# Performance work log

Hardware: AMD Instinct MI355X
Metric: run time of the kernel (lower is better)

The kernel has to match this reference:

```python
import jax, jax.numpy as jnp
import numpy as np

RES = 14          # window resolution -> N = RES*RES = 196
NUM_HEADS = 24
HEAD_DIM = 32
DIM = NUM_HEADS * HEAD_DIM  # 768
CPB_HIDDEN = 512
BATCH = 128


def _swin2_table_index(res):
    """Swin-v2 continuous relative position bias: log-spaced coords table
    [(2r-1)^2, 2] and relative position index [N*N] (numpy, static)."""
    r = res
    coords = np.arange(-(r - 1), r, dtype=np.float32)
    table = np.stack(np.meshgrid(coords, coords, indexing="ij"), axis=-1)  # [2r-1, 2r-1, 2]
    table = table / (r - 1)  # pretrained_window_size == window_size
    table = table * 8.0
    table = np.sign(table) * np.log2(np.abs(table) + 1.0) / np.log2(8.0)
    table = table.reshape(-1, 2)

    grid = np.stack(np.meshgrid(np.arange(r), np.arange(r), indexing="ij"))  # [2, r, r]
    grid = grid.reshape(2, -1)  # [2, N]
    rel = grid[:, :, None] - grid[:, None, :]  # [2, N, N]
    rel = rel.transpose(1, 2, 0).astype(np.int64)  # [N, N, 2]
    rel[..., 0] += r - 1
    rel[..., 1] += r - 1
    rel[..., 0] *= 2 * r - 1
    index = rel.sum(-1).reshape(-1)  # [N*N]
    return table, index


def setup_inputs() -> dict:
    key = jax.random.key(0)
    ks = jax.random.split(key, 5)
    N = RES * RES
    x = jax.random.normal(ks[0], (BATCH, N, DIM), dtype=jnp.float32)
    qkv_w = jax.random.normal(ks[1], (DIM, 3 * DIM), dtype=jnp.float32) * (DIM ** -0.5)
    qkv_b = jnp.zeros((3 * DIM,), dtype=jnp.float32)
    proj_w = jax.random.normal(ks[2], (DIM, DIM), dtype=jnp.float32) * (DIM ** -0.5)
    proj_b = jnp.zeros((DIM,), dtype=jnp.float32)
    cpb_w1 = jax.random.normal(ks[3], (2, CPB_HIDDEN), dtype=jnp.float32) * (2 ** -0.5)
    cpb_b1 = jnp.zeros((CPB_HIDDEN,), dtype=jnp.float32)
    cpb_w2 = jax.random.normal(ks[4], (CPB_HIDDEN, NUM_HEADS), dtype=jnp.float32) * (CPB_HIDDEN ** -0.5)
    cpb_b2 = jnp.zeros((NUM_HEADS,), dtype=jnp.float32)
    return {"x": x, "qkv_w": qkv_w, "qkv_b": qkv_b, "proj_w": proj_w,
            "proj_b": proj_b, "cpb_w1": cpb_w1, "cpb_b1": cpb_b1,
            "cpb_w2": cpb_w2, "cpb_b2": cpb_b2}


def reference(x, qkv_w, qkv_b, proj_w, proj_b, cpb_w1, cpb_b1, cpb_w2, cpb_b2):
    B, N, C = x.shape
    H, hd = NUM_HEADS, HEAD_DIM

    table_np, index_np = _swin2_table_index(RES)
    table = jnp.asarray(table_np)            # [(2r-1)^2, 2]
    index = jnp.asarray(index_np)            # [N*N] int

    # qkv projection -> (3, B, H, N, hd)
    qkv = x @ qkv_w + qkv_b
    qkv = qkv.reshape(B, N, 3, H, hd).transpose(2, 0, 3, 1, 4)
    q, k, v = qkv[0], qkv[1], qkv[2]

    # scaled QK^T
    attn = jnp.einsum("bhnd,bhmd->bhnm", q, k) / jnp.sqrt(jnp.float32(hd))

    # continuous relative position bias: MLP(2->512->H), gather, 16*sigmoid
    h1 = jax.nn.relu(table @ cpb_w1 + cpb_b1)           # [(2r-1)^2, 512]
    bias_table = h1 @ cpb_w2 + cpb_b2                    # [(2r-1)^2, H]
    bias = bias_table[index].reshape(N, N, H).transpose(2, 0, 1)  # [H, N, N]
    bias = 16.0 * jax.nn.sigmoid(bias)

    attn = jax.nn.softmax(attn + bias[None], axis=-1)

    out = jnp.einsum("bhnm,bhmd->bhnd", attn, v)
    out = out.transpose(0, 2, 1, 3).reshape(B, N, C)
    out = out @ proj_w + proj_b
    return out
```

## Files before the change

kernel.cpp:

```cpp
#include <hip/hip_runtime.h>
#include <hip/hip_bf16.h>

typedef unsigned short u16;
typedef __attribute__((ext_vector_type(8))) short short8;
typedef __attribute__((ext_vector_type(8))) u16 u16x8;
typedef __attribute__((ext_vector_type(4))) u16 u16x4;
typedef __attribute__((ext_vector_type(4))) float f32x4;

__device__ __forceinline__ u16 f2bf(float f) {
  __hip_bfloat16 h = __float2bfloat16(f);
  u16 u;
  __builtin_memcpy(&u, &h, 2);
  return u;
}

__device__ __forceinline__ f32x4 mfma16(short8 a, short8 b, f32x4 c) {
  return __builtin_amdgcn_mfma_f32_16x16x32_bf16(a, b, c, 0, 0, 0);
}

__device__ __forceinline__ void gl_lds16(const void* g, void* l) {
  __builtin_amdgcn_global_load_lds(
      (const __attribute__((address_space(1))) unsigned int*)g,
      (__attribute__((address_space(3))) unsigned int*)l, 16, 0, 0);
}

__global__ __launch_bounds__(256) void cvt_x_k(const float* __restrict__ x,
                                               u16* __restrict__ xb) {
  int i = (blockIdx.x * 256 + threadIdx.x) * 4;
  float4 v = *(const float4*)(x + i);
  u16x4 o = { f2bf(v.x), f2bf(v.y), f2bf(v.z), f2bf(v.w) };
  *(u16x4*)(xb + i) = o;
}

__global__ __launch_bounds__(256) void cvt_wt_k(const float* __restrict__ w,
                                                u16* __restrict__ wt, int N) {
  int i = blockIdx.x * 256 + threadIdx.x;
  int nn = i / 768, kk = i % 768;
  wt[i] = f2bf(w[(size_t)kk * N + nn]);
}

__device__ __forceinline__ float cpb_coord(int v) {
  float c = (float)(v - 13) * (8.0f / 13.0f);
  float a = fabsf(c);
  float r = log2f(a + 1.0f) * (1.0f / 3.0f);
  return c < 0.f ? -r : r;
}

__global__ __launch_bounds__(64) void bias_mlp_k(
    const float* __restrict__ w1, const float* __restrict__ b1,
    const float* __restrict__ w2, const float* __restrict__ b2,
    float* __restrict__ btab) {
  int e = blockIdx.x;
  int lane = threadIdx.x;
  float t0 = cpb_coord(e / 27), t1 = cpb_coord(e % 27);
  float acc[24];
#pragma unroll
  for (int hh = 0; hh < 24; hh++) acc[hh] = 0.f;
#pragma unroll
  for (int jj = 0; jj < 8; jj++) {
    int j = lane * 8 + jj;
    float h1 = t0 * w1[j] + t1 * w1[512 + j] + b1[j];
    h1 = fmaxf(h1, 0.f);
#pragma unroll
    for (int hh = 0; hh < 24; hh++) acc[hh] += h1 * w2[j * 24 + hh];
  }
#pragma unroll
  for (int hh = 0; hh < 24; hh++)
#pragma unroll
    for (int m = 1; m < 64; m <<= 1) acc[hh] += __shfl_xor(acc[hh], m, 64);
  if (lane == 0) {
#pragma unroll
    for (int hh = 0; hh < 24; hh++) {
      float v = acc[hh] + b2[hh];
      btab[e * 24 + hh] = 16.f / (1.f + __expf(-v));
    }
  }
}

__global__ __launch_bounds__(256) void bias_expand_k(const float* __restrict__ tab,
                                                     float* __restrict__ be) {
  int i = blockIdx.x * 256 + threadIdx.x;
  int h = i / (196 * 208);
  int rem = i % (196 * 208);
  int row = rem / 208, col = rem % 208;
  float v = 0.f;
  if (col < 196) {
    int dy = row / 14 - col / 14 + 13;
    int dx = row % 14 - col % 14 + 13;
    v = tab[(dy * 27 + dx) * 24 + h];
  }
  be[i] = v;
}

template <int EPI>
__global__ __launch_bounds__(256) void gemm_k(
    const u16* __restrict__ A, const u16* __restrict__ Bt,
    const float* __restrict__ bias, float* __restrict__ Cf,
    u16* __restrict__ Cb, int N, int K, int nbx) {
  __shared__ u16 As[128 * 64];
  __shared__ u16 Bs[128 * 64];
  const int tid = threadIdx.x, lane = tid & 63, w = tid >> 6;
  const int r16 = lane & 15, q4 = lane >> 4;
  const int wr = w >> 1, wc = w & 1;
  const int nwg = gridDim.x, cpx = nwg >> 3;
  const int swz = (blockIdx.x & 7) * cpx + (blockIdx.x >> 3);
  const int m0 = (swz / nbx) * 128, n0 = (swz % nbx) * 128;

  f32x4 acc[4][4] = {};

  for (int k0 = 0; k0 < K; k0 += 64) {
#pragma unroll
    for (int g = 0; g < 4; g++) {
      int chunk = (w * 4 + g) * 64 + lane;
      int row = chunk >> 3, p = chunk & 7;
      int gch = p ^ (row & 7);
      gl_lds16(A + (size_t)(m0 + row) * K + k0 + gch * 8, (char*)As + (w * 4 + g) * 1024);
      gl_lds16(Bt + (size_t)(n0 + row) * K + k0 + gch * 8, (char*)Bs + (w * 4 + g) * 1024);
    }
    __syncthreads();
#pragma unroll
    for (int kk = 0; kk < 2; kk++) {
      short8 af[4], bfr[4];
#pragma unroll
      for (int i = 0; i < 4; i++) {
        int row = wr * 64 + i * 16 + r16;
        int pc = (kk * 4 + q4) ^ (r16 & 7);
        af[i] = *(const short8*)((const char*)As + row * 128 + pc * 16);
      }
#pragma unroll
      for (int j = 0; j < 4; j++) {
        int row = wc * 64 + j * 16 + r16;
        int pc = (kk * 4 + q4) ^ (r16 & 7);
        bfr[j] = *(const short8*)((const char*)Bs + row * 128 + pc * 16);
      }
#pragma unroll
      for (int i = 0; i < 4; i++)
#pragma unroll
        for (int j = 0; j < 4; j++) acc[i][j] = mfma16(af[i], bfr[j], acc[i][j]);
    }
    __syncthreads();
  }

  const int nb = n0 + wc * 64 + r16;
  float bn[4];
#pragma unroll
  for (int j = 0; j < 4; j++) bn[j] = bias[nb + j * 16];
#pragma unroll
  for (int i = 0; i < 4; i++) {
#pragma unroll
    for (int r = 0; r < 4; r++) {
      int m = m0 + wr * 64 + i * 16 + q4 * 4 + r;
      if (EPI == 1) {
        float* cp = Cf + (size_t)m * N + nb;
#pragma unroll
        for (int j = 0; j < 4; j++) cp[j * 16] = acc[i][j][r] + bn[j];
      } else {
        u16* cp = Cb + (size_t)m * N + nb;
#pragma unroll
        for (int j = 0; j < 4; j++) cp[j * 16] = f2bf(acc[i][j][r] + bn[j]);
      }
    }
  }
}

__global__ __launch_bounds__(256) void attn_k(
    const u16* __restrict__ qkv, const float* __restrict__ be,
    u16* __restrict__ ao) {
  constexpr int PST = 232, VST = 232;
  __shared__ u16 Ks[208 * 32];
  __shared__ u16 Vt[32 * VST];
  __shared__ u16 Ps[4][16 * PST];
  const int tid = threadIdx.x, lane = tid & 63, w = tid >> 6;
  const int r16 = lane & 15, q4 = lane >> 4;
  const int bh = blockIdx.x, b = bh / 24, h = bh % 24;
  const u16* qp = qkv + (size_t)(b * 196) * 2304 + h * 32;
  const u16* kp = qp + 768;
  const u16* vp = qp + 1536;
  const float* bp = be + h * (196 * 208);
  const int ksw = (q4 ^ ((r16 >> 1) & 3)) * 16;

  for (int g = w; g < 13; g += 4) {
    int chunk = g * 64 + lane;
    int row = chunk >> 2;
    int gch = (chunk & 3) ^ ((row >> 1) & 3);
    gl_lds16(kp + (size_t)row * 2304 + gch * 8, (char*)Ks + g * 1024);
  }
  for (int c = tid; c < 784; c += 256) {
    int n = c >> 2, d0 = (c & 3) * 8;
    u16x8 vv = *(const u16x8*)(vp + (size_t)n * 2304 + (c & 3) * 8);
#pragma unroll
    for (int jj = 0; jj < 8; jj++) Vt[(d0 + jj) * VST + n] = vv[jj];
  }
  for (int idx = tid; idx < 32 * 36; idx += 256) {
    int d = idx / 36, n = 196 + idx % 36;
    Vt[d * VST + n] = 0;
  }
  for (int idx = lane; idx < 16 * 24; idx += 64) {
    int row = idx / 24, col = 208 + idx % 24;
    Ps[w][row * PST + col] = 0;
  }
  __syncthreads();

  f32x4 z = {0.f, 0.f, 0.f, 0.f};
  for (int si = w; si < 13; si += 4) {
    short8 aq = *(const short8*)(qp + (size_t)(si * 16 + r16) * 2304 + q4 * 8);
    f32x4 acc[13];
#pragma unroll
    for (int t = 0; t < 13; t++) {
      short8 bk = *(const short8*)((const char*)Ks + (t * 16 + r16) * 64 + ksw);
      acc[t] = mfma16(aq, bk, z);
    }
    float mx[4] = {-3e38f, -3e38f, -3e38f, -3e38f};
#pragma unroll
    for (int t = 0; t < 13; t++) {
      int col = t * 16 + r16;
#pragma unroll
      for (int r = 0; r < 4; r++) {
        int grow = si * 16 + q4 * 4 + r;
        int gc = grow < 196 ? grow : 195;
        float s = acc[t][r] * 0.17677669529663687f + bp[gc * 208 + col];
        s = (col < 196) ? s : -3e38f;
        acc[t][r] = s;
        mx[r] = fmaxf(mx[r], s);
      }
    }
#pragma unroll
    for (int r = 0; r < 4; r++)
#pragma unroll
      for (int m = 1; m < 16; m <<= 1) mx[r] = fmaxf(mx[r], __shfl_xor(mx[r], m, 64));
    float sum[4] = {0.f, 0.f, 0.f, 0.f};
#pragma unroll
    for (int t = 0; t < 13; t++)
#pragma unroll
      for (int r = 0; r < 4; r++) {
        float p = __expf(acc[t][r] - mx[r]);
        acc[t][r] = p;
        sum[r] += p;
      }
#pragma unroll
    for (int r = 0; r < 4; r++) {
#pragma unroll
      for (int m = 1; m < 16; m <<= 1) sum[r] += __shfl_xor(sum[r], m, 64);
      sum[r] = 1.0f / sum[r];
    }
#pragma unroll
    for (int t = 0; t < 13; t++) {
      int col = t * 16 + r16;
#pragma unroll
      for (int r = 0; r < 4; r++)
        Ps[w][(q4 * 4 + r) * PST + col] = f2bf(acc[t][r] * sum[r]);
    }
    f32x4 o0 = z, o1 = z;
#pragma unroll
    for (int t = 0; t < 7; t++) {
      short8 ap = *(const short8*)(&Ps[w][r16 * PST + t * 32 + q4 * 8]);
      short8 b0 = *(const short8*)(&Vt[r16 * VST + t * 32 + q4 * 8]);
      short8 b1 = *(const short8*)(&Vt[(16 + r16) * VST + t * 32 + q4 * 8]);
      o0 = mfma16(ap, b0, o0);
      o1 = mfma16(ap, b1, o1);
    }
#pragma unroll
    for (int r = 0; r < 4; r++) {
      int grow = si * 16 + q4 * 4 + r;
      if (grow < 196) {
        u16* op = ao + ((size_t)(b * 196 + grow)) * 768 + h * 32;
        op[r16] = f2bf(o0[r]);
        op[16 + r16] = f2bf(o1[r]);
      }
    }
  }
}

extern "C" void kernel_launch(void* const* d_in, const int* in_sizes, int n_in,
                              void* d_out, int out_size, void* d_ws, size_t ws_size,
                              hipStream_t stream) {
  const float* x = (const float*)d_in[0];
  const float* qkv_w = (const float*)d_in[1];
  const float* qkv_b = (const float*)d_in[2];
  const float* proj_w = (const float*)d_in[3];
  const float* proj_b = (const float*)d_in[4];
  const float* cpb_w1 = (const float*)d_in[5];
  const float* cpb_b1 = (const float*)d_in[6];
  const float* cpb_w2 = (const float*)d_in[7];
  const float* cpb_b2 = (const float*)d_in[8];
  float* out = (float*)d_out;

  char* ws = (char*)d_ws;
  size_t o = 0;
  auto alloc = [&](size_t sz) {
    size_t r = o;
    o = (o + sz + 255) & ~(size_t)255;
    return r;
  };
  const size_t ME = (size_t)25088 * 768;
  u16* x_bf = (u16*)(ws + alloc(ME * 2));
  u16* wq_t = (u16*)(ws + alloc((size_t)2304 * 768 * 2));
  u16* wp_t = (u16*)(ws + alloc((size_t)768 * 768 * 2));
  u16* qkv_s = (u16*)(ws + alloc(3 * ME * 2));
  float* btab = (float*)(ws + alloc((size_t)729 * 24 * 4));
  float* bexp = (float*)(ws + alloc((size_t)24 * 196 * 208 * 4));
  u16* ao = x_bf;

  cvt_x_k<<<18816, 256, 0, stream>>>(x, x_bf);
  cvt_wt_k<<<6912, 256, 0, stream>>>(qkv_w, wq_t, 2304);
  cvt_wt_k<<<2304, 256, 0, stream>>>(proj_w, wp_t, 768);
  bias_mlp_k<<<729, 64, 0, stream>>>(cpb_w1, cpb_b1, cpb_w2, cpb_b2, btab);
  bias_expand_k<<<3822, 256, 0, stream>>>(btab, bexp);
  gemm_k<0><<<3528, 256, 0, stream>>>(x_bf, wq_t, qkv_b, nullptr, qkv_s,
                                      2304, 768, 18);
  attn_k<<<3072, 256, 0, stream>>>(qkv_s, bexp, ao);
  gemm_k<1><<<1176, 256, 0, stream>>>(ao, wp_t, proj_b, out, nullptr,
                                      768, 768, 6);
}
```

Baseline: 314.7 us.

## Keep softmax probabilities in registers via transposed QK^T and 16x16x16 MFMA for PV

The QK^T MFMA now computes S^T by swapping the operands, so each lane holds four consecutive key columns of one query row. The probabilities can then be fed directly as the A operand of 16x16x16 bf16 MFMAs for the PV product, which removes the per-wave LDS staging buffer and its round trip. The bias is pre-scaled by log2(e) so softmax uses exp2, the row reductions need only two shuffles, bias reads become float4 loads, and the attention kernel gets an occupancy hint in its launch bounds. The trade-offs are twice as many, smaller MFMAs for PV and a changed V padding stride, and the asm fallback for the MFMA builtin may be fragile.

```diff
diff --git a/kernel.cpp b/kernel.cpp
--- a/kernel.cpp
+++ b/kernel.cpp
@@ -3,6 +3,7 @@
 
 typedef unsigned short u16;
 typedef __attribute__((ext_vector_type(8))) short short8;
+typedef __attribute__((ext_vector_type(4))) short short4v;
 typedef __attribute__((ext_vector_type(8))) u16 u16x8;
 typedef __attribute__((ext_vector_type(4))) u16 u16x4;
 typedef __attribute__((ext_vector_type(4))) float f32x4;
@@ -16,6 +17,15 @@
 
 __device__ __forceinline__ f32x4 mfma16(short8 a, short8 b, f32x4 c) {
   return __builtin_amdgcn_mfma_f32_16x16x32_bf16(a, b, c, 0, 0, 0);
+}
+
+__device__ __forceinline__ f32x4 mfma16x16(short4v a, short4v b, f32x4 c) {
+#if __has_builtin(__builtin_amdgcn_mfma_f32_16x16x16bf16_1k)
+  return __builtin_amdgcn_mfma_f32_16x16x16bf16_1k(a, b, c, 0, 0, 0);
+#else
+  asm("v_mfma_f32_16x16x16_bf16 %0, %1, %2, %0" : "+v"(c) : "v"(a), "v"(b));
+  return c;
+#endif
 }
 
 __device__ __forceinline__ void gl_lds16(const void* g, void* l) {
@@ -87,7 +97,7 @@
   if (col < 196) {
     int dy = row / 14 - col / 14 + 13;
     int dx = row % 14 - col % 14 + 13;
-    v = tab[(dy * 27 + dx) * 24 + h];
+    v = tab[(dy * 27 + dx) * 24 + h] * 1.4426950408889634f;
   }
   be[i] = v;
 }
@@ -163,13 +173,12 @@
   }
 }
 
-__global__ __launch_bounds__(256) void attn_k(
+__global__ __launch_bounds__(256, 4) void attn_k(
     const u16* __restrict__ qkv, const float* __restrict__ be,
     u16* __restrict__ ao) {
-  constexpr int PST = 232, VST = 232;
+  constexpr int VST = 236;
   __shared__ u16 Ks[208 * 32];
   __shared__ u16 Vt[32 * VST];
-  __shared__ u16 Ps[4][16 * PST];
   const int tid = threadIdx.x, lane = tid & 63, w = tid >> 6;
   const int r16 = lane & 15, q4 = lane >> 4;
   const int bh = blockIdx.x, b = bh / 24, h = bh % 24;
@@ -178,6 +187,7 @@
   const u16* vp = qp + 1536;
   const float* bp = be + h * (196 * 208);
   const int ksw = (q4 ^ ((r16 >> 1) & 3)) * 16;
+  const float SC2 = 0.17677669529663687f * 1.4426950408889634f;
 
   for (int g = w; g < 13; g += 4) {
     int chunk = g * 64 + lane;
@@ -191,73 +201,60 @@
 #pragma unroll
     for (int jj = 0; jj < 8; jj++) Vt[(d0 + jj) * VST + n] = vv[jj];
   }
-  for (int idx = tid; idx < 32 * 36; idx += 256) {
-    int d = idx / 36, n = 196 + idx % 36;
+  for (int idx = tid; idx < 32 * 40; idx += 256) {
+    int d = idx / 40, n = 196 + idx % 40;
     Vt[d * VST + n] = 0;
   }
-  for (int idx = lane; idx < 16 * 24; idx += 64) {
-    int row = idx / 24, col = 208 + idx % 24;
-    Ps[w][row * PST + col] = 0;
-  }
   __syncthreads();
 
-  f32x4 z = {0.f, 0.f, 0.f, 0.f};
+  const f32x4 z = {0.f, 0.f, 0.f, 0.f};
   for (int si = w; si < 13; si += 4) {
-    short8 aq = *(const short8*)(qp + (size_t)(si * 16 + r16) * 2304 + q4 * 8);
-    f32x4 acc[13];
+    short8 bq = *(const short8*)(qp + (size_t)(si * 16 + r16) * 2304 + q4 * 8);
+    f32x4 p[13];
 #pragma unroll
     for (int t = 0; t < 13; t++) {
-      short8 bk = *(const short8*)((const char*)Ks + (t * 16 + r16) * 64 + ksw);
-      acc[t] = mfma16(aq, bk, z);
-    }
-    float mx[4] = {-3e38f, -3e38f, -3e38f, -3e38f};
+      short8 ka = *(const short8*)((const char*)Ks + (t * 16 + r16) * 64 + ksw);
+      p[t] = mfma16(ka, bq, z);
+    }
+    int gc = si * 16 + r16;
+    gc = gc < 196 ? gc : 195;
+    const float* brow = bp + gc * 208 + q4 * 4;
+    float mx = -3e38f;
 #pragma unroll
     for (int t = 0; t < 13; t++) {
-      int col = t * 16 + r16;
+      float4 bv = *(const float4*)(brow + t * 16);
+      int k0 = t * 16 + q4 * 4;
+      p[t][0] = (k0 + 0 < 196) ? p[t][0] * SC2 + bv.x : -3e38f;
+      p[t][1] = (k0 + 1 < 196) ? p[t][1] * SC2 + bv.y : -3e38f;
+      p[t][2] = (k0 + 2 < 196) ? p[t][2] * SC2 + bv.z : -3e38f;
+      p[t][3] = (k0 + 3 < 196) ? p[t][3] * SC2 + bv.w : -3e38f;
+      mx = fmaxf(mx, fmaxf(fmaxf(p[t][0], p[t][1]), fmaxf(p[t][2], p[t][3])));
+    }
+    mx = fmaxf(mx, __shfl_xor(mx, 16, 64));
+    mx = fmaxf(mx, __shfl_xor(mx, 32, 64));
+    float sum = 0.f;
+#pragma unroll
+    for (int t = 0; t < 13; t++)
 #pragma unroll
       for (int r = 0; r < 4; r++) {
-        int grow = si * 16 + q4 * 4 + r;
-        int gc = grow < 196 ? grow : 195;
-        float s = acc[t][r] * 0.17677669529663687f + bp[gc * 208 + col];
-        s = (col < 196) ? s : -3e38f;
-        acc[t][r] = s;
-        mx[r] = fmaxf(mx[r], s);
-      }
-    }
-#pragma unroll
-    for (int r = 0; r < 4; r++)
-#pragma unroll
-      for (int m = 1; m < 16; m <<= 1) mx[r] = fmaxf(mx[r], __shfl_xor(mx[r], m, 64));
-    float sum[4] = {0.f, 0.f, 0.f, 0.f};
-#pragma unroll
-    for (int t = 0; t < 13; t++)
-#pragma unroll
-      for (int r = 0; r < 4; r++) {
-        float p = __expf(acc[t][r] - mx[r]);
-        acc[t][r] = p;
-        sum[r] += p;
-      }
-#pragma unroll
-    for (int r = 0; r < 4; r++) {
-#pragma unroll
-      for (int m = 1; m < 16; m <<= 1) sum[r] += __shfl_xor(sum[r], m, 64);
-      sum[r] = 1.0f / sum[r];
-    }
+        float e = __builtin_amdgcn_exp2f(p[t][r] - mx);
+        p[t][r] = e;
+        sum += e;
+      }
+    sum += __shfl_xor(sum, 16, 64);
+    sum += __shfl_xor(sum, 32, 64);
+    float rs = 1.0f / sum;
+    f32x4 o0 = z, o1 = z;
 #pragma unroll
     for (int t = 0; t < 13; t++) {
-      int col = t * 16 + r16;
-#pragma unroll
-      for (int r = 0; r < 4; r++)
-        Ps[w][(q4 * 4 + r) * PST + col] = f2bf(acc[t][r] * sum[r]);
-    }
-    f32x4 o0 = z, o1 = z;
-#pragma unroll
-    for (int t = 0; t < 7; t++) {
-      short8 ap = *(const short8*)(&Ps[w][r16 * PST + t * 32 + q4 * 8]);
-      short8 b0 = *(const short8*)(&Vt[r16 * VST + t * 32 + q4 * 8]);
-      short8 b1 = *(const short8*)(&Vt[(16 + r16) * VST + t * 32 + q4 * 8]);
-      o0 = mfma16(ap, b0, o0);
-      o1 = mfma16(ap, b1, o1);
+      short4v pa;
+#pragma unroll
+      for (int r = 0; r < 4; r++) pa[r] = (short)f2bf(p[t][r] * rs);
+      const u16* vrow = &Vt[r16 * VST + t * 16 + q4 * 4];
+      short4v b0 = *(const short4v*)vrow;
+      short4v b1 = *(const short4v*)(vrow + 16 * VST);
+      o0 = mfma16x16(pa, b0, o0);
+      o1 = mfma16x16(pa, b1, o1);
     }
 #pragma unroll
     for (int r = 0; r < 4; r++) {
```

Measured after the change: 454.4 us. 44.4% more time.
